# Kernel optimization log

Measured on AMD Instinct MI355X. Metric: run time of the kernel, lower is better.

Reference implementation:

```python
import jax, jax.numpy as jnp
import numpy as np

HEAD_DIM = 128
N_HEADS = 32
ROPE_DIM = 64
TOPK = 1024
B, S, HID, QLORA = 1, 2048, 4096, 1536
LN_EPS = 1e-5  # torch nn.LayerNorm default


def _hadamard_matrix(n):
    H = np.array([[1.0]], dtype=np.float32)
    while H.shape[0] < n:
        H = np.block([[H, H], [H, -H]])
    return jnp.asarray(H)

_H128 = _hadamard_matrix(HEAD_DIM)
_FWHT_SCALE = HEAD_DIM ** -0.5


def rotate_activation(x):
    # Fast Walsh-Hadamard transform == x @ H_sylvester, scaled by dim**-0.5
    return (x @ _H128) * _FWHT_SCALE


def rope_non_interleaved(x, cos, sin):
    # x: [..., rope_dim]; cos/sin: broadcastable [..., rope_dim/2]
    half = x.shape[-1] // 2
    x1, x2 = x[..., :half], x[..., half:]
    return jnp.concatenate([x1 * cos - x2 * sin, x1 * sin + x2 * cos], axis=-1)


def setup_inputs() -> dict:
    key = jax.random.key(0)
    ks = jax.random.split(key, 8)
    hidden_states = jax.random.normal(ks[0], (B, S, HID), jnp.float32)
    q_compressed = jax.random.normal(ks[1], (B, S, QLORA), jnp.float32)
    # rotary cos/sin for rope_dim=64 (standard concat layout)
    pos = jnp.arange(S, dtype=jnp.float32)
    inv_freq = 1.0 / (10000.0 ** (jnp.arange(0, ROPE_DIM, 2, dtype=jnp.float32) / ROPE_DIM))
    ang = pos[:, None] * inv_freq[None, :]  # [S, 32]
    cos = jnp.tile(jnp.cos(ang), (1, 2))[None]  # [1, S, 64]
    sin = jnp.tile(jnp.sin(ang), (1, 2))[None]
    # additive causal mask [B, S, S]
    causal = jnp.tril(jnp.ones((S, S), jnp.bool_))
    attention_mask = jnp.where(causal, 0.0, -1e9).astype(jnp.float32)[None]
    Wq_b = jax.random.normal(ks[2], (QLORA, N_HEADS * HEAD_DIM), jnp.float32) * (QLORA ** -0.5)
    Wk = jax.random.normal(ks[3], (HID, HEAD_DIM), jnp.float32) * (HID ** -0.5)
    k_gamma = jnp.ones((HEAD_DIM,), jnp.float32)
    k_beta = jnp.zeros((HEAD_DIM,), jnp.float32)
    Ww = jax.random.normal(ks[4], (HID, N_HEADS), jnp.float32) * (HID ** -0.5)
    return {"hidden_states": hidden_states, "q_compressed": q_compressed, "cos": cos,
            "sin": sin, "attention_mask": attention_mask, "Wq_b": Wq_b, "Wk": Wk,
            "k_gamma": k_gamma, "k_beta": k_beta, "Ww": Ww}


def reference(hidden_states, q_compressed, cos, sin, attention_mask, Wq_b, Wk, k_gamma, k_beta, Ww):
    b, s, _ = hidden_states.shape
    softmax_scale = HEAD_DIM ** -0.5
    # queries: [b, s, H, D]
    q = (q_compressed @ Wq_b).reshape(b, s, N_HEADS, HEAD_DIM)
    q_rope, q_nope = q[..., :ROPE_DIM], q[..., ROPE_DIM:]
    # keys: single shared head, LayerNorm(k)
    k = hidden_states @ Wk  # [b, s, D]
    mu = jnp.mean(k, axis=-1, keepdims=True)
    var = jnp.mean(jnp.square(k - mu), axis=-1, keepdims=True)
    k = (k - mu) * jax.lax.rsqrt(var + LN_EPS) * k_gamma + k_beta
    k_rope, k_nope = k[..., :ROPE_DIM], k[..., ROPE_DIM:]
    # non-interleaved RoPE (cos/sin truncated to half_dim=32)
    half = ROPE_DIM // 2
    c, sn = cos[..., :half], sin[..., :half]
    q_rope = rope_non_interleaved(q_rope, c[:, :, None, :], sn[:, :, None, :])
    k_rope = rope_non_interleaved(k_rope, c, sn)
    q = jnp.concatenate([q_rope, q_nope], axis=-1)
    k = jnp.concatenate([k_rope, k_nope], axis=-1)
    # Hadamard activation rotation
    q = rotate_activation(q)
    k = rotate_activation(k)
    # I_{t,s} = sum_h w_{t,h} * ReLU(q_{t,h} . k_s) * scale
    scores = jax.nn.relu(jnp.einsum('bthd,bsd->bths', q, k)) * softmax_scale
    weights = hidden_states @ Ww  # [b, t, H]
    index_scores = jnp.einsum('bths,bth->bts', scores, weights)
    index_scores = index_scores + attention_mask
    topk = min(TOPK, s)
    _, topk_indices = jax.lax.top_k(index_scores, topk)  # [b, s, topk]
    return topk_indices, index_scores
```

## Files before the change

kernel.cpp:

```cpp
#include <hip/hip_runtime.h>
#include <stdint.h>

#define S_LEN 2048
#define HID 4096
#define QLORA 1536
#define NH 32
#define HD 128
#define TOPK_N 1024
#define NEG_INF -1000000000.0f
#define INV_SQRT_HD 0.08838834764831844f

typedef __attribute__((ext_vector_type(8))) short short8;
typedef __attribute__((ext_vector_type(4))) short short4_;
typedef __attribute__((ext_vector_type(4))) float float4_;
typedef __attribute__((ext_vector_type(4))) unsigned uint4_;
typedef __attribute__((ext_vector_type(4))) int int4_;
typedef __attribute__((ext_vector_type(2))) int int2_;

__device__ __forceinline__ short f2bf(float x) {
  union { float f; unsigned u; } v; v.f = x;
  unsigned r = v.u + 0x7FFFu + ((v.u >> 16) & 1u);
  return (short)(r >> 16);
}

__device__ __forceinline__ unsigned f2ord(float x) {
  union { float f; unsigned u; } v; v.f = x;
  return v.u ^ (0x80000000u | (unsigned)((int)v.u >> 31));
}

__device__ __forceinline__ void gload_lds16(const void* g, void* l) {
  __builtin_amdgcn_global_load_lds((const __attribute__((address_space(1))) unsigned int*)g,
                                   (__attribute__((address_space(3))) unsigned int*)l, 16, 0, 0);
}

__global__ __launch_bounds__(256) void prep_kernel(
    const float* __restrict__ hidden, short* __restrict__ hidb,
    const float* __restrict__ qc, char* __restrict__ qc8,
    float* __restrict__ kacc,
    const float* __restrict__ wqb, char* __restrict__ wq8T,
    const float* __restrict__ wk, const float* __restrict__ ww,
    short* __restrict__ kwT) {
  __shared__ __align__(8) char stile[4352];
  int bid = blockIdx.x;
  const int tid = threadIdx.x;
  if (bid < 8192) {
    int i = bid * 256 + tid;
    float4 v = ((const float4*)hidden)[i];
    short4_ o;
    o[0] = f2bf(v.x); o[1] = f2bf(v.y); o[2] = f2bf(v.z); o[3] = f2bf(v.w);
    ((short4_*)hidb)[i] = o;
    return;
  }
  if (bid < 9728) {
    int i = (bid - 8192) * 256 + tid;
    float4 f0 = ((const float4*)qc)[i * 2];
    float4 f1 = ((const float4*)qc)[i * 2 + 1];
    int lo = 0, hi = 0;
    lo = __builtin_amdgcn_cvt_pk_fp8_f32(f0.x, f0.y, lo, 0);
    lo = __builtin_amdgcn_cvt_pk_fp8_f32(f0.z, f0.w, lo, 1);
    hi = __builtin_amdgcn_cvt_pk_fp8_f32(f1.x, f1.y, hi, 0);
    hi = __builtin_amdgcn_cvt_pk_fp8_f32(f1.z, f1.w, hi, 1);
    ((int2_*)qc8)[i] = (int2_){lo, hi};
    return;
  }
  if (bid < 10048) {
    int i = (bid - 9728) * 256 + tid;
    ((float4_*)kacc)[i] = (float4_){0.f, 0.f, 0.f, 0.f};
    return;
  }
  if (bid < 13120) {
    char (*t8)[33] = (char(*)[33])stile;
    int b = bid - 10048;
    int k0 = (b >> 7) * 64, n0 = (b & 127) * 32;
    #pragma unroll
    for (int i = 0; i < 8; i++) {
      int e = tid + i * 256;
      int r = e >> 5, c = e & 31;
      float x = wqb[(size_t)(k0 + r) * HID + n0 + c];
      t8[r][c] = (char)__builtin_amdgcn_cvt_pk_fp8_f32(x, x, 0, 0);
    }
    __syncthreads();
    int nl = tid >> 3, jk = (tid & 7) * 8;
    union { char c[8]; long l; } o;
    #pragma unroll
    for (int j = 0; j < 8; j++) o.c[j] = t8[jk + j][nl];
    *(long*)(wq8T + (size_t)(n0 + nl) * QLORA + k0 + jk) = o.l;
    return;
  }
  short (*tile)[33] = (short(*)[33])stile;
  const float* in; short* out; int R, C, bx, by;
  if (bid < 13632) {
    int b2 = bid - 13120;
    in = wk; out = kwT; R = HID; C = HD; bx = b2 & 3; by = b2 >> 2;
  } else {
    int b3 = bid - 13632;
    in = ww; out = kwT + 128 * HID; R = HID; C = NH; bx = 0; by = b3;
  }
  int c0 = bx * 32, r0 = by * 32;
  int tx = tid & 31, ty = tid >> 5;
  #pragma unroll
  for (int i = 0; i < 32; i += 8)
    tile[ty + i][tx] = f2bf(in[(size_t)(r0 + ty + i) * C + c0 + tx]);
  __syncthreads();
  #pragma unroll
  for (int i = 0; i < 32; i += 8)
    out[(size_t)(c0 + ty + i) * R + r0 + tx] = tile[tx][ty + i];
}

#define QSTAGE8(kt, Ad, Bd) do { \
  _Pragma("unroll") \
  for (int i = 0; i < 4; i++) { \
    int m = w * 32 + i * 8 + lr; \
    int gb = (kt) * 128 + ((lc ^ (m & 7)) << 4); \
    gload_lds16(qc8 + (size_t)(t0 + m) * QLORA + gb, (Ad) + (w * 32 + i * 8) * 128); \
    gload_lds16(wq8T + (size_t)(n0 + m) * QLORA + gb, (Bd) + (w * 32 + i * 8) * 128); \
  } \
} while (0)

#define QCOMPUTE8(Aq, Bq) do { \
  _Pragma("unroll") \
  for (int p = 0; p < 4; p++) { \
    int ch = p * 2 + (quad >> 1); \
    int lo8 = (quad & 1) * 8; \
    long a[2], b[8]; \
    _Pragma("unroll") \
    for (int mt = 0; mt < 2; mt++) { \
      int m = w * 32 + mt * 16 + l15; \
      a[mt] = *(const long*)((Aq) + m * 128 + ((ch ^ (m & 7)) << 4) + lo8); \
    } \
    _Pragma("unroll") \
    for (int nt = 0; nt < 8; nt++) { \
      int n = nt * 16 + l15; \
      b[nt] = *(const long*)((Bq) + n * 128 + ((ch ^ (n & 7)) << 4) + lo8); \
    } \
    _Pragma("unroll") \
    for (int mt = 0; mt < 2; mt++) \
      _Pragma("unroll") \
      for (int nt = 0; nt < 8; nt++) \
        acc[mt][nt] = __builtin_amdgcn_mfma_f32_16x16x32_fp8_fp8(a[mt], b[nt], acc[mt][nt], 0, 0, 0); \
  } \
} while (0)

__global__ __launch_bounds__(256, 4) void gemms_kernel(
    const char* __restrict__ qc8, const char* __restrict__ wq8T,
    const float* __restrict__ cosp, const float* __restrict__ sinp,
    short* __restrict__ qrot,
    const short* __restrict__ hidb, const short* __restrict__ kwT,
    float* __restrict__ kacc) {
  __shared__ __align__(16) char smem[32768];
  const int tid = threadIdx.x;
  const int w = tid >> 6, lane = tid & 63;
  const int l15 = lane & 15, quad = lane >> 4;
  const int lr = lane >> 3, lc = lane & 7;

  if (blockIdx.x < 512) {
    char* A0 = smem;
    char* B0 = smem + 16384;
    const int n0 = (blockIdx.x & 31) * 128;
    const int t0 = (blockIdx.x >> 5) * 128;

    float4_ acc[2][8];
    #pragma unroll
    for (int mt = 0; mt < 2; mt++)
      #pragma unroll
      for (int i = 0; i < 8; i++) acc[mt][i] = (float4_){0.f, 0.f, 0.f, 0.f};

    QSTAGE8(0, A0, B0);
    __syncthreads();
    for (int kt = 0; ; kt++) {
      QCOMPUTE8(A0, B0);
      if (kt == 11) break;
      __syncthreads();
      QSTAGE8(kt + 1, A0, B0);
      __syncthreads();
    }

    #pragma unroll
    for (int mt = 0; mt < 2; mt++) {
      #pragma unroll
      for (int r = 0; r < 4; r++) {
        const int trow = t0 + w * 32 + mt * 16 + quad * 4 + r;
        float v[8];
        #pragma unroll
        for (int nt = 0; nt < 8; nt++) v[nt] = acc[mt][nt][r];
        float cc0 = cosp[trow * 64 + l15], cc1 = cosp[trow * 64 + 16 + l15];
        float ss0 = sinp[trow * 64 + l15], ss1 = sinp[trow * 64 + 16 + l15];
        float r0 = v[0] * cc0 - v[2] * ss0, r1 = v[1] * cc1 - v[3] * ss1;
        float r2 = v[0] * ss0 + v[2] * cc0, r3 = v[1] * ss1 + v[3] * cc1;
        v[0] = r0; v[1] = r1; v[2] = r2; v[3] = r3;
        short* orow = qrot + (size_t)trow * HID + n0;
        #pragma unroll
        for (int nt = 0; nt < 8; nt++)
          orow[nt * 16 + l15] = f2bf(v[nt]);
      }
    }
  } else {
    short* Al = (short*)smem;
    short* Bl = (short*)(smem + 8192);
    const int b2 = blockIdx.x - 512;
    const int kc0 = (b2 & 7) * 512;
    const int m0g = (b2 >> 3) * 64;

    float4_ acc[10];
    #pragma unroll
    for (int i = 0; i < 10; i++) acc[i] = (float4_){0.f, 0.f, 0.f, 0.f};

    for (int k0 = kc0; k0 < kc0 + 512; k0 += 64) {
      #pragma unroll
      for (int i = 0; i < 2; i++) {
        int m = w * 16 + i * 8 + lr;
        int gk = k0 + ((lc ^ (m & 7)) << 3);
        gload_lds16(hidb + (size_t)(m0g + m) * HID + gk, Al + (w * 16 + i * 8) * 64);
      }
      #pragma unroll
      for (int i = 0; i < 5; i++) {
        int n = w * 40 + i * 8 + lr;
        int gk = k0 + ((lc ^ (n & 7)) << 3);
        gload_lds16(kwT + (size_t)n * HID + gk, Bl + (w * 40 + i * 8) * 64);
      }
      __syncthreads();
      #pragma unroll
      for (int kk = 0; kk < 64; kk += 32) {
        int ca = (kk >> 3) + quad;
        int ma = w * 16 + l15;
        short8 a = *(const short8*)(Al + ma * 64 + ((ca ^ (ma & 7)) << 3));
        #pragma unroll
        for (int nt = 0; nt < 10; nt++) {
          int n = nt * 16 + l15;
          short8 b = *(const short8*)(Bl + n * 64 + ((ca ^ (n & 7)) << 3));
          acc[nt] = __builtin_amdgcn_mfma_f32_16x16x32_bf16(a, b, acc[nt], 0, 0, 0);
        }
      }
      __syncthreads();
    }
    #pragma unroll
    for (int nt = 0; nt < 10; nt++)
      #pragma unroll
      for (int r = 0; r < 4; r++) {
        int row = m0g + w * 16 + quad * 4 + r;
        atomicAdd(&kacc[(size_t)row * 160 + nt * 16 + l15], acc[nt][r]);
      }
  }
}

__global__ __launch_bounds__(256) void ln_rope_kernel(
    const float* __restrict__ kacc, const float* __restrict__ gamma,
    const float* __restrict__ beta, const float* __restrict__ cosp,
    const float* __restrict__ sinp, short* __restrict__ krot) {
  const int tid = threadIdx.x;
  const int row = blockIdx.x * 16 + (tid >> 4);
  const int l16 = tid & 15;
  const int c0 = l16 * 8;
  const float* rp = kacc + (size_t)row * 160 + c0;
  float4 f0 = ((const float4*)rp)[0], f1 = ((const float4*)rp)[1];
  float v[8] = {f0.x, f0.y, f0.z, f0.w, f1.x, f1.y, f1.z, f1.w};
  float s = 0.f, ss = 0.f;
  #pragma unroll
  for (int j = 0; j < 8; j++) { s += v[j]; ss += v[j] * v[j]; }
  #pragma unroll
  for (int d = 1; d <= 8; d <<= 1) {
    s += __shfl_xor(s, d, 64); ss += __shfl_xor(ss, d, 64);
  }
  float mu = s * (1.0f / 128.0f);
  float var = ss * (1.0f / 128.0f) - mu * mu;
  float rs = rsqrtf(var + 1e-5f);
  #pragma unroll
  for (int j = 0; j < 8; j++)
    v[j] = (v[j] - mu) * rs * gamma[c0 + j] + beta[c0 + j];
  #pragma unroll
  for (int j = 0; j < 8; j++) {
    float p = __shfl_xor(v[j], 4, 64);
    if (l16 < 8) {
      int idx = (c0 + j) & 31;
      float c = cosp[row * 64 + idx], sn = sinp[row * 64 + idx];
      v[j] = v[j] * c + p * ((l16 < 4) ? -sn : sn);
    }
  }
  short8 o;
  #pragma unroll
  for (int j = 0; j < 8; j++) o[j] = f2bf(v[j]);
  *(short8*)(krot + (size_t)row * 128 + c0) = o;
}

__global__ __launch_bounds__(256, 2) void scores_kernel(
    const short* __restrict__ qrot, const short* __restrict__ krot,
    const float* __restrict__ kacc, float* __restrict__ isc) {
  __shared__ __align__(16) char smem[65536];
  short* buf0 = (short*)smem;
  short* buf1 = (short*)(smem + 32768);

  const int tid = threadIdx.x;
  const int w = tid >> 6, lane = tid & 63;
  const int l15 = lane & 15, quad = lane >> 4;
  const int wm = w >> 1, wn = w & 1;
  const int lr16 = lane >> 4, lc16 = lane & 15;

  const int bid = blockIdx.x;
  const int strip = (bid & 1) ? (511 - (bid >> 1)) : (bid >> 1);
  const int t0 = strip * 4;
  const int nsb = (t0 + 3) / 128 + 1;

  const short* Abase = qrot + (size_t)t0 * 32 * 128;
  #pragma unroll
  for (int i = 0; i < 8; i++) {
    int m = (w * 8 + i) * 4 + lr16;
    int gofs = m * 128 + ((lc16 ^ (m & 7)) << 3);
    gload_lds16(Abase + gofs, buf0 + (w * 8 + i) * 512);
    gload_lds16(krot + gofs, buf1 + (w * 8 + i) * 512);
  }
  __syncthreads();

  short8 af[4][4];
  #pragma unroll
  for (int k4 = 0; k4 < 4; k4++) {
    int ca = k4 * 4 + quad;
    #pragma unroll
    for (int mt = 0; mt < 4; mt++) {
      int m = wm * 64 + mt * 16 + l15;
      af[k4][mt] = *(const short8*)(buf0 + m * 128 + ((ca ^ (m & 7)) << 3));
    }
  }

  const int t_a = t0 + wm * 2, t_b = t_a + 1;
  float wq[4][4];
  #pragma unroll
  for (int mt = 0; mt < 4; mt++) {
    int tt = (mt < 2) ? t_a : t_b;
    #pragma unroll
    for (int r = 0; r < 4; r++)
      wq[mt][r] = kacc[(size_t)tt * 160 + 128 + (mt & 1) * 16 + quad * 4 + r];
  }
  __syncthreads();

  for (int sb = 0; sb < nsb; sb++) {
    short* cur = (sb & 1) ? buf0 : buf1;
    if (sb + 1 < nsb) {
      short* nxt = (sb & 1) ? buf1 : buf0;
      const short* Bbase = krot + (size_t)(sb + 1) * 128 * 128;
      #pragma unroll
      for (int i = 0; i < 8; i++) {
        int m = (w * 8 + i) * 4 + lr16;
        int gofs = m * 128 + ((lc16 ^ (m & 7)) << 3);
        gload_lds16(Bbase + gofs, nxt + (w * 8 + i) * 512);
      }
    }

    float4_ acc[4][4];
    #pragma unroll
    for (int mt = 0; mt < 4; mt++)
      #pragma unroll
      for (int nt = 0; nt < 4; nt++) acc[mt][nt] = (float4_){0.f, 0.f, 0.f, 0.f};

    #pragma unroll
    for (int k4 = 0; k4 < 4; k4++) {
      int ca = k4 * 4 + quad;
      short8 b[4];
      #pragma unroll
      for (int nt = 0; nt < 4; nt++) {
        int n = wn * 64 + nt * 16 + l15;
        b[nt] = *(const short8*)(cur + n * 128 + ((ca ^ (n & 7)) << 3));
      }
      #pragma unroll
      for (int mt = 0; mt < 4; mt++)
        #pragma unroll
        for (int nt = 0; nt < 4; nt++)
          acc[mt][nt] = __builtin_amdgcn_mfma_f32_16x16x32_bf16(af[k4][mt], b[nt], acc[mt][nt], 0, 0, 0);
    }

    #pragma unroll
    for (int nt = 0; nt < 4; nt++) {
      float pa = 0.f, pb = 0.f;
      #pragma unroll
      for (int r = 0; r < 4; r++) {
        pa += fmaxf(acc[0][nt][r], 0.f) * wq[0][r] + fmaxf(acc[1][nt][r], 0.f) * wq[1][r];
        pb += fmaxf(acc[2][nt][r], 0.f) * wq[2][r] + fmaxf(acc[3][nt][r], 0.f) * wq[3][r];
      }
      pa += __shfl_xor(pa, 16, 64); pa += __shfl_xor(pa, 32, 64);
      pb += __shfl_xor(pb, 16, 64); pb += __shfl_xor(pb, 32, 64);
      int s = sb * 128 + wn * 64 + nt * 16 + l15;
      if (quad == 0)
        isc[(size_t)t_a * S_LEN + s] = (s <= t_a) ? pa * INV_SQRT_HD : NEG_INF;
      else if (quad == 1)
        isc[(size_t)t_b * S_LEN + s] = (s <= t_b) ? pb * INV_SQRT_HD : NEG_INF;
    }

    __syncthreads();
  }

  if (wn == 0) {
    const int myrow = (lane < 32) ? t_a : t_b;
    const int l32 = lane & 31;
    float4_ nf = (float4_){NEG_INF, NEG_INF, NEG_INF, NEG_INF};
    float4_* rowp = (float4_*)(isc + (size_t)myrow * S_LEN);
    for (int i = nsb * 32 + l32; i < 512; i += 32) rowp[i] = nf;
  }
}


__device__ __forceinline__ void ce(unsigned &a, unsigned &b, bool d) {
  unsigned mx = a > b ? a : b;
  unsigned mn = a > b ? b : a;
  a = d ? mx : mn;
  b = d ? mn : mx;
}

__device__ __forceinline__ void mtop3(unsigned* v, bool d) {
  #pragma unroll
  for (int j = 16; j >= 4; j >>= 1)
    #pragma unroll
    for (int r = 0; r < 32; ++r)
      if (!(r & j)) ce(v[r], v[r ^ j], d);
}

template <int JT>
__device__ __forceinline__ void mreg(unsigned* v, bool d) {
  #pragma unroll
  for (int j = JT; j >= 1; j >>= 1)
    #pragma unroll
    for (int r = 0; r < 32; ++r)
      if (!(r & j)) ce(v[r], v[r ^ j], d);
}

#define IDX_L0   ((l << 5) | (q << 2))
#define IDX_654  (((l >> 2) << 7) | (q << 4) | ((l & 3) << 2))
#define IDX_765  (((l >> 3) << 8) | (q << 5) | ((l & 7) << 2))
#define IDX_876  (((l >> 4) << 9) | (q << 6) | ((l & 15) << 2))
#define IDX_543  (((l >> 1) << 6) | (q << 3) | ((l & 1) << 2))
#define IDX_987  (((l >> 5) << 10) | (q << 7) | ((l & 31) << 2))
#define IDX_1098 ((q << 8) | (l << 2))
#define SWZW(ix) ((ix) ^ ((((ix) >> 5) & 7) << 2))

#define RT(FROM, TO) do {                                               \
  _Pragma("unroll")                                                     \
  for (int q = 0; q < 8; ++q) {                                         \
    int ix = (FROM);                                                    \
    *(uint4_*)(buf + SWZW(ix)) =                                        \
        (uint4_){v[4 * q], v[4 * q + 1], v[4 * q + 2], v[4 * q + 3]};   \
  }                                                                     \
  _Pragma("unroll")                                                     \
  for (int q = 0; q < 8; ++q) {                                         \
    int ix = (TO);                                                      \
    uint4_ u = *(const uint4_*)(buf + SWZW(ix));                        \
    v[4 * q] = u[0]; v[4 * q + 1] = u[1];                               \
    v[4 * q + 2] = u[2]; v[4 * q + 3] = u[3];                           \
  }                                                                     \
} while (0)

__global__ __launch_bounds__(256) void topk_kernel(const float* __restrict__ isc,
                                                   int* __restrict__ idx_out) {
  __shared__ __align__(16) unsigned sbuf[4][2048];
  const int tid = threadIdx.x;
  const int w = tid >> 6, l = tid & 63;
  unsigned* buf = sbuf[w];
  const int gid = blockIdx.x * 4 + w;
  const bool shortrow = (gid < 512);
  int trow, sbase;
  if (shortrow) { trow = gid * 2 + (l >> 5); sbase = (l & 31) << 5; }
  else          { trow = 512 + gid;          sbase = l << 5; }

  unsigned v[32];
  {
    const float* rp = isc + (size_t)trow * S_LEN + sbase;
    #pragma unroll
    for (int g = 0; g < 8; ++g) {
      float4 f = ((const float4*)rp)[g];
      unsigned b0 = (unsigned)(2047 - (sbase + g * 4));
      v[g * 4 + 0] = (f2ord(f.x) & 0xFFFFF800u) | b0;
      v[g * 4 + 1] = (f2ord(f.y) & 0xFFFFF800u) | (b0 - 1);
      v[g * 4 + 2] = (f2ord(f.z) & 0xFFFFF800u) | (b0 - 2);
      v[g * 4 + 3] = (f2ord(f.w) & 0xFFFFF800u) | (b0 - 3);
    }
  }

  #pragma unroll
  for (int r = 0; r < 32; r += 2) ce(v[r], v[r + 1], ((r & 2) == 0));
  #pragma unroll
  for (int j = 2; j >= 1; j >>= 1)
    #pragma unroll
    for (int r = 0; r < 32; ++r)
      if (!(r & j)) ce(v[r], v[r ^ j], ((r & 4) == 0));
  #pragma unroll
  for (int j = 4; j >= 1; j >>= 1)
    #pragma unroll
    for (int r = 0; r < 32; ++r)
      if (!(r & j)) ce(v[r], v[r ^ j], ((r & 8) == 0));
  #pragma unroll
  for (int j = 8; j >= 1; j >>= 1)
    #pragma unroll
    for (int r = 0; r < 32; ++r)
      if (!(r & j)) ce(v[r], v[r ^ j], ((r & 16) == 0));

  mreg<16>(v, (l & 1) == 0);

  {
    bool d = ((l & 2) == 0);
    bool keep = (((l & 1) == 0) == d);
    #pragma unroll
    for (int r = 0; r < 32; ++r) {
      unsigned pv = (unsigned)__shfl_xor((int)v[r], 1, 64);
      unsigned mx = v[r] > pv ? v[r] : pv;
      unsigned mn = v[r] > pv ? pv : v[r];
      v[r] = keep ? mx : mn;
    }
    mreg<16>(v, d);
  }

  {
    bool d = ((l & 4) == 0);
    RT(IDX_L0, IDX_654);  mtop3(v, d);
    RT(IDX_654, IDX_L0);  mreg<8>(v, d);
  }
  {
    bool d = ((l & 8) == 0);
    RT(IDX_L0, IDX_765);  mtop3(v, d);
    RT(IDX_765, IDX_L0);  mreg<16>(v, d);
  }
  {
    bool d = ((l & 16) == 0);
    RT(IDX_L0, IDX_876);  mtop3(v, d);
    RT(IDX_876, IDX_543); mtop3(v, d);
    RT(IDX_543, IDX_L0);  mreg<4>(v, d);
  }
  {
    bool d = shortrow ? true : (l < 32);
    RT(IDX_L0, IDX_987);  mtop3(v, d);
    RT(IDX_987, IDX_654); mtop3(v, d);
    RT(IDX_654, IDX_L0);  mreg<8>(v, d);
  }
  if (!shortrow) {
    RT(IDX_L0, IDX_1098); mtop3(v, true);
    RT(IDX_1098, IDX_765); mtop3(v, true);
    RT(IDX_765, IDX_L0);  mreg<16>(v, true);
  }

  if (shortrow || l < 32) {
    int* op = idx_out + (size_t)trow * TOPK_N + sbase;
    #pragma unroll
    for (int g = 0; g < 8; ++g) {
      int4_ o;
      #pragma unroll
      for (int j = 0; j < 4; ++j) o[j] = 2047 - (int)(v[g * 4 + j] & 0x7FFu);
      ((int4_*)op)[g] = o;
    }
  }
}

extern "C" void kernel_launch(void* const* d_in, const int* in_sizes, int n_in,
                              void* d_out, int out_size, void* d_ws, size_t ws_size,
                              hipStream_t stream) {
  const float* hidden = (const float*)d_in[0];
  const float* qc     = (const float*)d_in[1];
  const float* cosp   = (const float*)d_in[2];
  const float* sinp   = (const float*)d_in[3];
  const float* wqb    = (const float*)d_in[5];
  const float* wk     = (const float*)d_in[6];
  const float* gamma  = (const float*)d_in[7];
  const float* beta   = (const float*)d_in[8];
  const float* ww     = (const float*)d_in[9];

  char* ws = (char*)d_ws;
  short* hidb = (short*)ws;
  char*  qc8  = (char*)(ws + 16777216);
  char*  wq8T = (char*)(ws + 19922944);
  short* kwT  = (short*)(ws + 26214400);
  short* krot = (short*)(ws + 27525120);
  short* qrot = (short*)(ws + 28049408);
  float* kacc = (float*)(ws + 44826624);

  int*   idx_out = (int*)d_out;
  float* isc     = ((float*)d_out) + (size_t)S_LEN * TOPK_N;

  prep_kernel<<<dim3(13760), dim3(256), 0, stream>>>(hidden, hidb, qc, qc8, kacc,
                                                     wqb, wq8T, wk, ww, kwT);
  gemms_kernel<<<dim3(768), dim3(256), 0, stream>>>(qc8, wq8T, cosp, sinp, qrot,
                                                    hidb, kwT, kacc);
  ln_rope_kernel<<<dim3(128), dim3(256), 0, stream>>>(kacc, gamma, beta, cosp, sinp, krot);
  scores_kernel<<<dim3(512), dim3(256), 0, stream>>>(qrot, krot, kacc, isc);
  topk_kernel<<<dim3(384), dim3(256), 0, stream>>>(isc, idx_out);
}
```

Measured before the change: 226.2 us.

## Split scores kernel key blocks across two workgroups, single-buffer LDS for occupancy

The scores kernel now launches two workgroups per 4-row query strip, each handling alternating 128-key blocks (even or odd), which doubles the grid. The LDS double buffer is replaced with a single 32KB buffer and launch bounds raised to four blocks per CU. The aim is to shorten the long causal strips' critical path and raise occupancy, at the cost of losing in-block prefetch overlap and loading the Q tile twice.

```diff
diff --git a/kernel.cpp b/kernel.cpp
--- a/kernel.cpp
+++ b/kernel.cpp
@@ -282,12 +282,11 @@
   *(short8*)(krot + (size_t)row * 128 + c0) = o;
 }
 
-__global__ __launch_bounds__(256, 2) void scores_kernel(
+__global__ __launch_bounds__(256, 4) void scores_kernel(
     const short* __restrict__ qrot, const short* __restrict__ krot,
     const float* __restrict__ kacc, float* __restrict__ isc) {
-  __shared__ __align__(16) char smem[65536];
-  short* buf0 = (short*)smem;
-  short* buf1 = (short*)(smem + 32768);
+  __shared__ __align__(16) char smem[32768];
+  short* buf = (short*)smem;
 
   const int tid = threadIdx.x;
   const int w = tid >> 6, lane = tid & 63;
@@ -296,7 +295,8 @@
   const int lr16 = lane >> 4, lc16 = lane & 15;
 
   const int bid = blockIdx.x;
-  const int strip = (bid & 1) ? (511 - (bid >> 1)) : (bid >> 1);
+  const int pair = bid >> 1, half = bid & 1;
+  const int strip = (pair & 1) ? (511 - (pair >> 1)) : (pair >> 1);
   const int t0 = strip * 4;
   const int nsb = (t0 + 3) / 128 + 1;
 
@@ -305,8 +305,7 @@
   for (int i = 0; i < 8; i++) {
     int m = (w * 8 + i) * 4 + lr16;
     int gofs = m * 128 + ((lc16 ^ (m & 7)) << 3);
-    gload_lds16(Abase + gofs, buf0 + (w * 8 + i) * 512);
-    gload_lds16(krot + gofs, buf1 + (w * 8 + i) * 512);
+    gload_lds16(Abase + gofs, buf + (w * 8 + i) * 512);
   }
   __syncthreads();
 
@@ -317,7 +316,7 @@
     #pragma unroll
     for (int mt = 0; mt < 4; mt++) {
       int m = wm * 64 + mt * 16 + l15;
-      af[k4][mt] = *(const short8*)(buf0 + m * 128 + ((ca ^ (m & 7)) << 3));
+      af[k4][mt] = *(const short8*)(buf + m * 128 + ((ca ^ (m & 7)) << 3));
     }
   }
 
@@ -330,69 +329,79 @@
     for (int r = 0; r < 4; r++)
       wq[mt][r] = kacc[(size_t)tt * 160 + 128 + (mt & 1) * 16 + quad * 4 + r];
   }
-  __syncthreads();
-
-  for (int sb = 0; sb < nsb; sb++) {
-    short* cur = (sb & 1) ? buf0 : buf1;
-    if (sb + 1 < nsb) {
-      short* nxt = (sb & 1) ? buf1 : buf0;
-      const short* Bbase = krot + (size_t)(sb + 1) * 128 * 128;
-      #pragma unroll
-      for (int i = 0; i < 8; i++) {
-        int m = (w * 8 + i) * 4 + lr16;
-        int gofs = m * 128 + ((lc16 ^ (m & 7)) << 3);
-        gload_lds16(Bbase + gofs, nxt + (w * 8 + i) * 512);
-      }
-    }
-
-    float4_ acc[4][4];
-    #pragma unroll
-    for (int mt = 0; mt < 4; mt++)
-      #pragma unroll
-      for (int nt = 0; nt < 4; nt++) acc[mt][nt] = (float4_){0.f, 0.f, 0.f, 0.f};
-
-    #pragma unroll
-    for (int k4 = 0; k4 < 4; k4++) {
-      int ca = k4 * 4 + quad;
-      short8 b[4];
-      #pragma unroll
-      for (int nt = 0; nt < 4; nt++) {
-        int n = wn * 64 + nt * 16 + l15;
-        b[nt] = *(const short8*)(cur + n * 128 + ((ca ^ (n & 7)) << 3));
-      }
-      #pragma unroll
-      for (int mt = 0; mt < 4; mt++)
-        #pragma unroll
-        for (int nt = 0; nt < 4; nt++)
-          acc[mt][nt] = __builtin_amdgcn_mfma_f32_16x16x32_bf16(af[k4][mt], b[nt], acc[mt][nt], 0, 0, 0);
-    }
-
-    #pragma unroll
-    for (int nt = 0; nt < 4; nt++) {
-      float pa = 0.f, pb = 0.f;
-      #pragma unroll
-      for (int r = 0; r < 4; r++) {
-        pa += fmaxf(acc[0][nt][r], 0.f) * wq[0][r] + fmaxf(acc[1][nt][r], 0.f) * wq[1][r];
-        pb += fmaxf(acc[2][nt][r], 0.f) * wq[2][r] + fmaxf(acc[3][nt][r], 0.f) * wq[3][r];
-      }
-      pa += __shfl_xor(pa, 16, 64); pa += __shfl_xor(pa, 32, 64);
-      pb += __shfl_xor(pb, 16, 64); pb += __shfl_xor(pb, 32, 64);
-      int s = sb * 128 + wn * 64 + nt * 16 + l15;
-      if (quad == 0)
-        isc[(size_t)t_a * S_LEN + s] = (s <= t_a) ? pa * INV_SQRT_HD : NEG_INF;
-      else if (quad == 1)
-        isc[(size_t)t_b * S_LEN + s] = (s <= t_b) ? pb * INV_SQRT_HD : NEG_INF;
-    }
-
-    __syncthreads();
-  }
-
-  if (wn == 0) {
+
+  if (half == 0 && wn == 0) {
     const int myrow = (lane < 32) ? t_a : t_b;
     const int l32 = lane & 31;
     float4_ nf = (float4_){NEG_INF, NEG_INF, NEG_INF, NEG_INF};
     float4_* rowp = (float4_*)(isc + (size_t)myrow * S_LEN);
     for (int i = nsb * 32 + l32; i < 512; i += 32) rowp[i] = nf;
+  }
+  __syncthreads();
+
+  int sb = half;
+  if (sb < nsb) {
+    const int bw = (w * 8) * 4;
+    #pragma unroll
+    for (int i = 0; i < 8; i++) {
+      int m = (w * 8 + i) * 4 + lr16;
+      int gofs = m * 128 + ((lc16 ^ (m & 7)) << 3);
+      gload_lds16(krot + (size_t)sb * 128 * 128 + gofs, buf + (w * 8 + i) * 512);
+    }
+    __syncthreads();
+    for (;;) {
+      float4_ acc[4][4];
+      #pragma unroll
+      for (int mt = 0; mt < 4; mt++)
+        #pragma unroll
+        for (int nt = 0; nt < 4; nt++) acc[mt][nt] = (float4_){0.f, 0.f, 0.f, 0.f};
+
+      #pragma unroll
+      for (int k4 = 0; k4 < 4; k4++) {
+        int ca = k4 * 4 + quad;
+        short8 b[4];
+        #pragma unroll
+        for (int nt = 0; nt < 4; nt++) {
+          int n = wn * 64 + nt * 16 + l15;
+          b[nt] = *(const short8*)(buf + n * 128 + ((ca ^ (n & 7)) << 3));
+        }
+        #pragma unroll
+        for (int mt = 0; mt < 4; mt++)
+          #pragma unroll
+          for (int nt = 0; nt < 4; nt++)
+            acc[mt][nt] = __builtin_amdgcn_mfma_f32_16x16x32_bf16(af[k4][mt], b[nt], acc[mt][nt], 0, 0, 0);
+      }
+
+      #pragma unroll
+      for (int nt = 0; nt < 4; nt++) {
+        float pa = 0.f, pb = 0.f;
+        #pragma unroll
+        for (int r = 0; r < 4; r++) {
+          pa += fmaxf(acc[0][nt][r], 0.f) * wq[0][r] + fmaxf(acc[1][nt][r], 0.f) * wq[1][r];
+          pb += fmaxf(acc[2][nt][r], 0.f) * wq[2][r] + fmaxf(acc[3][nt][r], 0.f) * wq[3][r];
+        }
+        pa += __shfl_xor(pa, 16, 64); pa += __shfl_xor(pa, 32, 64);
+        pb += __shfl_xor(pb, 16, 64); pb += __shfl_xor(pb, 32, 64);
+        int s = sb * 128 + wn * 64 + nt * 16 + l15;
+        if (quad == 0)
+          isc[(size_t)t_a * S_LEN + s] = (s <= t_a) ? pa * INV_SQRT_HD : NEG_INF;
+        else if (quad == 1)
+          isc[(size_t)t_b * S_LEN + s] = (s <= t_b) ? pb * INV_SQRT_HD : NEG_INF;
+      }
+
+      int nx = sb + 2;
+      if (nx >= nsb) break;
+      __syncthreads();
+      #pragma unroll
+      for (int i = 0; i < 8; i++) {
+        int m = (w * 8 + i) * 4 + lr16;
+        int gofs = m * 128 + ((lc16 ^ (m & 7)) << 3);
+        gload_lds16(krot + (size_t)nx * 128 * 128 + gofs, buf + (w * 8 + i) * 512);
+      }
+      __syncthreads();
+      sb = nx;
+    }
+    (void)bw;
   }
 }
 
@@ -575,6 +584,6 @@
   gemms_kernel<<<dim3(768), dim3(256), 0, stream>>>(qc8, wq8T, cosp, sinp, qrot,
                                                     hidb, kwT, kacc);
   ln_rope_kernel<<<dim3(128), dim3(256), 0, stream>>>(kacc, gamma, beta, cosp, sinp, krot);
-  scores_kernel<<<dim3(512), dim3(256), 0, stream>>>(qrot, krot, kacc, isc);
+  scores_kernel<<<dim3(1024), dim3(256), 0, stream>>>(qrot, krot, kacc, isc);
   topk_kernel<<<dim3(384), dim3(256), 0, stream>>>(isc, idx_out);
 }
```

Measured after the change: 307.0 us. +35.7%, slower.
